# Optimization experiments

Measured on AMD Instinct MI355X. Metric: run time of the kernel, lower is better.

The kernel has to match this reference:

```python
import jax, jax.numpy as jnp
import numpy as np

NG, N, NFG, NFR, NFP, B = 4, 64, 1024, 256, 256, 2048
SCALE = 1.0 / float(np.sqrt(NFR + NFP))
EPS = 1e-5  # torch LayerNorm default


def setup_inputs() -> dict:
    key = jax.random.key(0)
    k = jax.random.split(key, 4)
    x = jax.random.normal(k[0], (B, N, NFG), dtype=jnp.float32)
    # per-graph params stacked over NG for vectorized computation
    Wt = jax.random.normal(k[1], (NG, NFR, NFG), dtype=jnp.float32) * 0.02
    bt = jnp.zeros((NG, NFR), dtype=jnp.float32)
    Wp = jax.random.normal(k[2], (NG, NFR, NFG), dtype=jnp.float32) * 0.02
    bp = jnp.zeros((NG, NFR), dtype=jnp.float32)
    Wg = jax.random.normal(k[3], (NG, NFG, NFG), dtype=jnp.float32) * 0.02  # [out,in]
    gamma = jnp.ones((NG, NFG), dtype=jnp.float32)
    beta = jnp.zeros((NG, NFG), dtype=jnp.float32)
    return {"x": x, "Wt": Wt, "bt": bt, "Wp": Wp, "bp": bp,
            "Wg": Wg, "gamma": gamma, "beta": beta}


def reference(x, Wt, bt, Wp, bp, Wg, gamma, beta):
    # theta/phi projections, vectorized over NG graphs: [G,B,N,R]
    theta = jnp.einsum('bnf,grf->gbnr', x, Wt) + bt[:, None, None, :]
    phi = jnp.einsum('bnf,grf->gbnr', x, Wp) + bp[:, None, None, :]
    # original computes sim=theta@phi^T then .sum(2); identical math:
    # relation[b,n] = theta[b,n] . sum_m phi[b,m]  (avoids the NxN matrix)
    phi_sum = phi.sum(axis=2)                                  # [G,B,R]
    relation = jnp.einsum('gbnr,gbr->gbn', theta, phi_sum) * SCALE
    w = jax.nn.softmax(relation, axis=2)                       # softmax over boxes N
    # attention-weighted aggregation over boxes -> [G,B,NFG]
    agg = jnp.einsum('gbn,bnf->gbf', w, x)
    # GCN linear (no bias): [G,B,NFG]
    h = jnp.einsum('gbf,gof->gbo', agg, Wg)
    # LayerNorm over feature dim, per graph
    mu = h.mean(axis=-1, keepdims=True)
    var = ((h - mu) ** 2).mean(axis=-1, keepdims=True)
    h = (h - mu) * jax.lax.rsqrt(var + EPS) * gamma[:, None, :] + beta[:, None, :]
    h = jax.nn.relu(h)
    # mean over the NG graphs; restore keepdim axis -> [B,1,NFG]
    return h.mean(axis=0)[:, None, :]
```

## Files before the change

### kernel.cpp

```cpp
#include <hip/hip_runtime.h>
#include <hip/hip_bf16.h>

typedef __attribute__((ext_vector_type(4))) float f4;
typedef __attribute__((ext_vector_type(4))) float f32x4;
typedef __attribute__((ext_vector_type(8))) short short8;
typedef __attribute__((ext_vector_type(2))) unsigned int u32x2;
typedef __attribute__((ext_vector_type(4))) unsigned int u32x4;
typedef unsigned int u32;
typedef unsigned short u16;

#define SCALE_F 0.04419417382415922f

__device__ inline u16 f2bf(float f) {
  u32 u = __float_as_uint(f);
  u32 r = u + 0x7FFFu + ((u >> 16) & 1u);
  return (u16)(r >> 16);
}
__device__ inline u32 pk(float a, float b) {
  return (u32)f2bf(a) | ((u32)f2bf(b) << 16);
}
__device__ inline float bflo(u32 u) { return __uint_as_float(u << 16); }
__device__ inline float bfhi(u32 u) { return __uint_as_float(u & 0xFFFF0000u); }

#define GLD16(gsrc, ldst)                                                     \
  __builtin_amdgcn_global_load_lds(                                           \
      (const __attribute__((address_space(1))) void*)(gsrc),                  \
      (__attribute__((address_space(3))) void*)(ldst), 16, 0, 0)

#define SWZ(o) (((o) & ~2047) | (((((o) >> 4) & 127) ^ (((o) >> 11) & 7)) << 4))

__device__ __forceinline__ void cvt8(const float* __restrict__ src,
                                     u16* __restrict__ dst, int blk, int t) {
  int i = blk * 256 + t;
  const f4* s = (const f4*)src;
  f4 a = s[(size_t)i * 2];
  f4 b = s[(size_t)i * 2 + 1];
  u32x4 p;
  p[0] = pk(a[0], a[1]);
  p[1] = pk(a[2], a[3]);
  p[2] = pk(b[0], b[1]);
  p[3] = pk(b[2], b[3]);
  *(u32x4*)(dst + (size_t)i * 8) = p;
}

__global__ __launch_bounds__(256) void k01_prep(const float* __restrict__ x,
                                                const float* __restrict__ Wg,
                                                const float* __restrict__ Wp,
                                                const float* __restrict__ Wt,
                                                u16* __restrict__ xs16,
                                                char* __restrict__ xpre,
                                                u16* __restrict__ wgb,
                                                u16* __restrict__ wpb,
                                                u16* __restrict__ wtb) {
  __shared__ float red[256][8];
  __shared__ u16 tile[64][66];
  const int blk = blockIdx.x, t = threadIdx.x;
  if (blk < 2048) {
    const int b = blk;
    const float* xb = x + (size_t)b * 65536;
    char* xp = xpre + (size_t)b * 131072;
    const int g16 = t & 127, rp = t >> 7;
    f4 acc0 = {0.f, 0.f, 0.f, 0.f}, acc1 = {0.f, 0.f, 0.f, 0.f};
#pragma unroll 8
    for (int it = 0; it < 32; ++it) {
      int n = it * 2 + rp;
      const float* src = xb + n * 1024 + g16 * 8;
      f4 v0 = *(const f4*)(src);
      f4 v1 = *(const f4*)(src + 4);
      acc0 += v0;
      acc1 += v1;
      u32x4 p;
      p[0] = pk(v0[0], v0[1]);
      p[1] = pk(v0[2], v0[3]);
      p[2] = pk(v1[0], v1[1]);
      p[3] = pk(v1[2], v1[3]);
      *(u32x4*)(xp + n * 2048 + g16 * 16) = p;
    }
    *(f4*)&red[t][0] = acc0;
    *(f4*)&red[t][4] = acc1;
    __syncthreads();
    if (t < 128) {
      f4 s0 = *(const f4*)&red[t][0];
      f4 s1 = *(const f4*)&red[t][4];
      f4 q0 = *(const f4*)&red[t + 128][0];
      f4 q1 = *(const f4*)&red[t + 128][4];
      s0 += q0;
      s1 += q1;
      u32x4 p;
      p[0] = pk(s0[0], s0[1]);
      p[1] = pk(s0[2], s0[3]);
      p[2] = pk(s1[0], s1[1]);
      p[3] = pk(s1[2], s1[3]);
      *(u32x4*)(xs16 + (size_t)b * 1024 + t * 8) = p;
    }
  } else if (blk < 4096) {
    cvt8(Wg, wgb, blk - 2048, t);
  } else if (blk < 4608) {
    cvt8(Wp, wpb, blk - 4096, t);
  } else {
    const int bid = blk - 4608;
    const int g = bid >> 6, rem = bid & 63;
    const int f0 = (rem & 15) * 64, r0 = (rem >> 4) * 64;
    const float* src = Wt + ((size_t)g * 256 + r0) * 1024 + f0;
#pragma unroll
    for (int i = 0; i < 16; ++i) {
      int idx = t + i * 256;
      int rl = idx >> 6, fl = idx & 63;
      tile[fl][rl] = f2bf(src[rl * 1024 + fl]);
    }
    __syncthreads();
    u16* dst = wtb + ((size_t)g * 1024 + f0) * 256 + r0;
#pragma unroll
    for (int i = 0; i < 4; ++i) {
      int idx = t + i * 256;
      int fl = idx >> 4, rq = idx & 15;
      u32x2 p;
      p[0] = (u32)tile[fl][rq * 4]     | ((u32)tile[fl][rq * 4 + 1] << 16);
      p[1] = (u32)tile[fl][rq * 4 + 2] | ((u32)tile[fl][rq * 4 + 3] << 16);
      *(u32x2*)(dst + fl * 256 + rq * 4) = p;
    }
  }
}

__global__ __launch_bounds__(256) void k2_gemm(const u16* __restrict__ A,
                                               const u16* __restrict__ Bt,
                                               const float* __restrict__ bp,
                                               u16* __restrict__ C) {
  const int n0 = blockIdx.x * 64, m0 = blockIdx.y * 128;
  __shared__ u16 Al[128 * 32];
  __shared__ u16 Bl[64 * 32];
  const int t = threadIdx.x;
  const int w = t >> 6, l = t & 63;
  const int lr = l & 15, lh = l >> 4;
  f32x4 acc[2][4] = {};
  for (int kt = 0; kt < 1024; kt += 32) {
#pragma unroll
    for (int j = 0; j < 2; ++j) {
      int idx = t + j * 256;
      int row = idx >> 2, sl = idx & 3;
      GLD16(A + (size_t)(m0 + row) * 1024 + kt + sl * 8, Al + idx * 8);
    }
    {
      int row = t >> 2, sl = t & 3;
      GLD16(Bt + (size_t)(n0 + row) * 1024 + kt + sl * 8, Bl + t * 8);
    }
    __syncthreads();
    short8 af[2], bfr[4];
#pragma unroll
    for (int m = 0; m < 2; ++m)
      af[m] = *(const short8*)(Al + (w * 32 + m * 16 + lr) * 32 + lh * 8);
#pragma unroll
    for (int n = 0; n < 4; ++n)
      bfr[n] = *(const short8*)(Bl + (n * 16 + lr) * 32 + lh * 8);
#pragma unroll
    for (int m = 0; m < 2; ++m)
#pragma unroll
      for (int n = 0; n < 4; ++n)
        acc[m][n] = __builtin_amdgcn_mfma_f32_16x16x32_bf16(af[m], bfr[n],
                                                            acc[m][n], 0, 0, 0);
    __syncthreads();
  }
#pragma unroll
  for (int m = 0; m < 2; ++m)
#pragma unroll
    for (int n = 0; n < 4; ++n) {
      int col = n0 + n * 16 + lr;
      float bb = 64.0f * bp[col];
#pragma unroll
      for (int j = 0; j < 4; ++j)
        C[(size_t)(m0 + w * 32 + m * 16 + lh * 4 + j) * 1024 + col] =
            f2bf(acc[m][n][j] + bb);
    }
}

__global__ __launch_bounds__(256) void k3_gemm(const u16* __restrict__ A,
                                               const u16* __restrict__ Btt,
                                               u16* __restrict__ Vb) {
  const int id = blockIdx.x;
  const int wg = (id & 7) * 64 + (id >> 3);
  const int n0 = (wg & 7) * 128, m0 = ((wg >> 3) & 15) * 128, g = wg >> 7;
  const u16* Bg = Btt + (size_t)g * 1024 * 256;
  __shared__ u16 Al[128 * 32];
  __shared__ u16 Bl[128 * 32];
  const int t = threadIdx.x;
  const int w = t >> 6, l = t & 63;
  const int wr = w >> 1, wc = w & 1;
  const int lr = l & 15, lh = l >> 4;
  f32x4 acc[4][4] = {};
  for (int kt = 0; kt < 256; kt += 32) {
#pragma unroll
    for (int j = 0; j < 2; ++j) {
      int idx = t + j * 256;
      int row = idx >> 2, sl = idx & 3;
      GLD16(A + (size_t)(m0 + row) * 1024 + g * 256 + kt + sl * 8, Al + idx * 8);
      GLD16(Bg + (size_t)(n0 + row) * 256 + kt + sl * 8, Bl + idx * 8);
    }
    __syncthreads();
    short8 af[4], bfr[4];
#pragma unroll
    for (int m = 0; m < 4; ++m)
      af[m] = *(const short8*)(Al + (wr * 64 + m * 16 + lr) * 32 + lh * 8);
#pragma unroll
    for (int n = 0; n < 4; ++n)
      bfr[n] = *(const short8*)(Bl + (wc * 64 + n * 16 + lr) * 32 + lh * 8);
#pragma unroll
    for (int m = 0; m < 4; ++m)
#pragma unroll
      for (int n = 0; n < 4; ++n)
        acc[m][n] = __builtin_amdgcn_mfma_f32_16x16x32_bf16(af[m], bfr[n],
                                                            acc[m][n], 0, 0, 0);
    __syncthreads();
  }
  u16* Vg = Vb + (size_t)g * 2048 * 1024;
#pragma unroll
  for (int m = 0; m < 4; ++m)
#pragma unroll
    for (int n = 0; n < 4; ++n)
#pragma unroll
      for (int j = 0; j < 4; ++j)
        Vg[(size_t)(m0 + wr * 64 + m * 16 + lh * 4 + j) * 1024 +
           (n0 + wc * 64 + n * 16 + lr)] = f2bf(acc[m][n][j]);
}

__device__ __forceinline__ void relation_phase(const char* xl, const u16* vb,
                                               float* relp, int w, int l) {
  const int lg = l >> 4, lr = l & 15;
  f32x4 racc[4] = {};
#pragma unroll
  for (int kp = 0; kp < 2; ++kp) {
    const int kt = kp * 512 + w * 32;
    short8 afr = {};
    if (lr < 4) afr = *(const short8*)(vb + lr * 1032 + kt + lg * 8);
#pragma unroll
    for (int nt = 0; nt < 4; ++nt) {
      int n = nt * 16 + lr;
      short8 bfrg = *(const short8*)(
          xl + n * 2048 + ((((kt >> 3) + lg) ^ (n & 7)) << 4));
      racc[nt] = __builtin_amdgcn_mfma_f32_16x16x32_bf16(afr, bfrg, racc[nt],
                                                         0, 0, 0);
    }
  }
  if (l < 16) {
#pragma unroll
    for (int nt = 0; nt < 4; ++nt)
#pragma unroll
      for (int j = 0; j < 4; ++j)
        relp[(w * 4 + j) * 64 + nt * 16 + lr] = racc[nt][j];
  }
}

__device__ __forceinline__ void softmax_phase(const float* relp, float* wsm,
                                              int t) {
  if (t < 256) {
    const int g = t >> 6, n = t & 63;
    float rel = 0.f;
#pragma unroll
    for (int ww = 0; ww < 16; ++ww) rel += relp[(ww * 4 + g) * 64 + n];
    rel *= SCALE_F;
    float mx = rel;
#pragma unroll
    for (int o = 32; o > 0; o >>= 1) mx = fmaxf(mx, __shfl_xor(mx, o, 64));
    float e = __expf(rel - mx);
    float s = e;
#pragma unroll
    for (int o = 32; o > 0; o >>= 1) s += __shfl_xor(s, o, 64);
    wsm[t] = e / s;
  }
}

__device__ __forceinline__ void agg_phase(const char* xl, const float* wsm,
                                          float* relp, u16* aggb, int b,
                                          int t) {
  const int hh = t >> 9, r = t & 511, g = r >> 7, f8 = r & 127;
  const float* wg = wsm + g * 64 + hh * 32;
  float a0 = 0, a1 = 0, a2 = 0, a3 = 0, a4 = 0, a5 = 0, a6 = 0, a7 = 0;
#pragma unroll 8
  for (int n0 = 0; n0 < 32; ++n0) {
    int n = hh * 32 + n0;
    float wv = wg[n0];
    u32x4 xp = *(const u32x4*)(xl + n * 2048 + ((f8 ^ (n & 7)) << 4));
    a0 = fmaf(bflo(xp[0]), wv, a0);
    a1 = fmaf(bfhi(xp[0]), wv, a1);
    a2 = fmaf(bflo(xp[1]), wv, a2);
    a3 = fmaf(bfhi(xp[1]), wv, a3);
    a4 = fmaf(bflo(xp[2]), wv, a4);
    a5 = fmaf(bfhi(xp[2]), wv, a5);
    a6 = fmaf(bflo(xp[3]), wv, a6);
    a7 = fmaf(bfhi(xp[3]), wv, a7);
  }
  if (hh) {
    f4 q0 = {a0, a1, a2, a3};
    f4 q1 = {a4, a5, a6, a7};
    *(f4*)(relp + r * 8) = q0;
    *(f4*)(relp + r * 8 + 4) = q1;
  }
  __syncthreads();
  if (!hh) {
    f4 q0 = *(const f4*)(relp + r * 8);
    f4 q1 = *(const f4*)(relp + r * 8 + 4);
    u32x4 p;
    p[0] = pk(a0 + q0[0], a1 + q0[1]);
    p[1] = pk(a2 + q0[2], a3 + q0[3]);
    p[2] = pk(a4 + q1[0], a5 + q1[1]);
    p[3] = pk(a6 + q1[2], a7 + q1[3]);
    *(u32x4*)(aggb + ((size_t)g * 2048 + b) * 1024 + f8 * 8) = p;
  }
}

#define K4_LDS (131072 + 8256 + 16384 + 1024)
__global__ __launch_bounds__(1024) void k4_fused(const char* __restrict__ xpre,
                                                 const u16* __restrict__ vb16,
                                                 u16* __restrict__ aggb) {
  extern __shared__ char sm[];
  char* xl = sm;
  u16* vb = (u16*)(sm + 131072);
  float* relp = (float*)(sm + 131072 + 8256);
  float* wsm = (float*)(sm + 131072 + 8256 + 16384);
  const int t = threadIdx.x;
  const int w = t >> 6, l = t & 63;
  const int bbase = (255 - (int)blockIdx.x) * 8;

  {
    int g = t >> 8, q = t & 255;
    u32x2 pv = *(const u32x2*)(vb16 + ((size_t)g * 2048 + bbase) * 1024 + q * 4);
    *(u32x2*)(vb + g * 1032 + q * 4) = pv;
  }
  const char* xg0 = xpre + (size_t)bbase * 131072;
#pragma unroll
  for (int i = 0; i < 8; ++i) {
    int o = (w * 8 + i) * 1024 + l * 16;
    GLD16(xg0 + SWZ(o), xl + o);
  }
  __syncthreads();

  u32x4 pf0, pf1, pf2, pf3, pf4, pf5, pf6, pf7;
  u32x2 pv1;
  for (int ib = 0; ib < 8; ++ib) {
    const int b = bbase + ib;
    if (ib < 7) {
      const char* xg1 = xpre + (size_t)(b + 1) * 131072;
      pf0 = *(const u32x4*)(xg1 + SWZ(t * 16));
      pf1 = *(const u32x4*)(xg1 + SWZ(t * 16 + 16384));
      pf2 = *(const u32x4*)(xg1 + SWZ(t * 16 + 32768));
      pf3 = *(const u32x4*)(xg1 + SWZ(t * 16 + 49152));
      pf4 = *(const u32x4*)(xg1 + SWZ(t * 16 + 65536));
      pf5 = *(const u32x4*)(xg1 + SWZ(t * 16 + 81920));
      pf6 = *(const u32x4*)(xg1 + SWZ(t * 16 + 98304));
      pf7 = *(const u32x4*)(xg1 + SWZ(t * 16 + 114688));
      pv1 = *(const u32x2*)(vb16 + ((size_t)(t >> 8) * 2048 + (b + 1)) * 1024 +
                            (t & 255) * 4);
    }
    relation_phase(xl, vb, relp, w, l);
    __syncthreads();
    softmax_phase(relp, wsm, t);
    __syncthreads();
    agg_phase(xl, wsm, relp, aggb, b, t);
    __syncthreads();
    if (ib < 7) {
      *(u32x4*)(xl + t * 16) = pf0;
      *(u32x4*)(xl + t * 16 + 16384) = pf1;
      *(u32x4*)(xl + t * 16 + 32768) = pf2;
      *(u32x4*)(xl + t * 16 + 49152) = pf3;
      *(u32x4*)(xl + t * 16 + 65536) = pf4;
      *(u32x4*)(xl + t * 16 + 81920) = pf5;
      *(u32x4*)(xl + t * 16 + 98304) = pf6;
      *(u32x4*)(xl + t * 16 + 114688) = pf7;
      *(u32x2*)(vb + (t >> 8) * 1032 + (t & 255) * 4) = pv1;
      __syncthreads();
    }
  }
}

__global__ __launch_bounds__(256) void k5_gemm(const u16* __restrict__ Ab,
                                               const u16* __restrict__ Bb,
                                               u16* __restrict__ H) {
  const int id = blockIdx.x;
  const int wg = (id & 7) * 64 + (id >> 3);
  const int n0 = (wg & 7) * 128, m0 = ((wg >> 3) & 15) * 128, g = wg >> 7;
  const u16* A = Ab + (size_t)g * 2048 * 1024;
  const u16* Bt = Bb + (size_t)g * 1024 * 1024;
  __shared__ u16 Al[128 * 32];
  __shared__ u16 Bl[128 * 32];
  const int t = threadIdx.x;
  const int w = t >> 6, l = t & 63;
  const int wr = w >> 1, wc = w & 1;
  const int lr = l & 15, lh = l >> 4;
  f32x4 acc[4][4] = {};
  for (int kt = 0; kt < 1024; kt += 32) {
#pragma unroll
    for (int j = 0; j < 2; ++j) {
      int idx = t + j * 256;
      int row = idx >> 2, sl = idx & 3;
      GLD16(A + (size_t)(m0 + row) * 1024 + kt + sl * 8, Al + idx * 8);
      GLD16(Bt + (size_t)(n0 + row) * 1024 + kt + sl * 8, Bl + idx * 8);
    }
    __syncthreads();
    short8 af[4], bfr[4];
#pragma unroll
    for (int m = 0; m < 4; ++m)
      af[m] = *(const short8*)(Al + (wr * 64 + m * 16 + lr) * 32 + lh * 8);
#pragma unroll
    for (int n = 0; n < 4; ++n)
      bfr[n] = *(const short8*)(Bl + (wc * 64 + n * 16 + lr) * 32 + lh * 8);
#pragma unroll
    for (int m = 0; m < 4; ++m)
#pragma unroll
      for (int n = 0; n < 4; ++n)
        acc[m][n] = __builtin_amdgcn_mfma_f32_16x16x32_bf16(af[m], bfr[n],
                                                            acc[m][n], 0, 0, 0);
    __syncthreads();
  }
  u16* Hg = H + (size_t)g * 2048 * 1024;
#pragma unroll
  for (int m = 0; m < 4; ++m)
#pragma unroll
    for (int n = 0; n < 4; ++n)
#pragma unroll
      for (int j = 0; j < 4; ++j)
        Hg[(size_t)(m0 + wr * 64 + m * 16 + lh * 4 + j) * 1024 +
           (n0 + wc * 64 + n * 16 + lr)] = f2bf(acc[m][n][j]);
}

__global__ __launch_bounds__(256) void k6_ln(const u16* __restrict__ H,
                                             const float* __restrict__ gamma,
                                             const float* __restrict__ beta,
                                             float* __restrict__ out) {
  const int b = blockIdx.x, t = threadIdx.x;
  const int w = t >> 6, lane = t & 63;
  __shared__ float red[8];
  f4 acc = {0.f, 0.f, 0.f, 0.f};
  for (int g = 0; g < 4; ++g) {
    u32x2 hp = *(const u32x2*)(H + ((size_t)g * 2048 + b) * 1024 + t * 4);
    f4 hv = {bflo(hp[0]), bfhi(hp[0]), bflo(hp[1]), bfhi(hp[1])};
    float s = hv[0] + hv[1] + hv[2] + hv[3];
    float q = hv[0] * hv[0] + hv[1] * hv[1] + hv[2] * hv[2] + hv[3] * hv[3];
#pragma unroll
    for (int o = 32; o > 0; o >>= 1) {
      s += __shfl_xor(s, o, 64);
      q += __shfl_xor(q, o, 64);
    }
    if (lane == 0) { red[w] = s; red[4 + w] = q; }
    __syncthreads();
    s = red[0] + red[1] + red[2] + red[3];
    q = red[4] + red[5] + red[6] + red[7];
    float mean = s * (1.f / 1024.f);
    float var = q * (1.f / 1024.f) - mean * mean;
    float rstd = rsqrtf(var + 1e-5f);
    f4 gm = *(const f4*)(gamma + g * 1024 + t * 4);
    f4 bt = *(const f4*)(beta + g * 1024 + t * 4);
#pragma unroll
    for (int j = 0; j < 4; ++j) {
      float val = (hv[j] - mean) * rstd * gm[j] + bt[j];
      acc[j] += fmaxf(val, 0.f);
    }
    __syncthreads();
  }
  acc *= 0.25f;
  *(f4*)(out + (size_t)b * 1024 + t * 4) = acc;
}

extern "C" void kernel_launch(void* const* d_in, const int* in_sizes, int n_in,
                              void* d_out, int out_size, void* d_ws, size_t ws_size,
                              hipStream_t stream) {
  const float* x     = (const float*)d_in[0];
  const float* Wt    = (const float*)d_in[1];
  const float* Wp    = (const float*)d_in[3];
  const float* bp    = (const float*)d_in[4];
  const float* Wg    = (const float*)d_in[5];
  const float* gamma = (const float*)d_in[6];
  const float* beta  = (const float*)d_in[7];
  float* out = (float*)d_out;

  char* ws = (char*)d_ws;
  u16*   xs16 = (u16*)(ws);
  u16*   ps16 = (u16*)(ws + (4u << 20));
  u16*   wpb  = (u16*)(ws + (8u << 20));
  u16*   wtb  = (u16*)(ws + (10u << 20));
  u16*   wgb  = (u16*)(ws + (12u << 20));
  u16*   vb16 = (u16*)(ws + (20u << 20));
  u16*   aggb = (u16*)(ws + (36u << 20));
  u16*   hb16 = (u16*)(ws + (52u << 20));
  char*  xpre = (char*)(ws + (68u << 20));

  hipFuncSetAttribute((const void*)k4_fused,
                      hipFuncAttributeMaxDynamicSharedMemorySize, K4_LDS);

  k01_prep<<<4864, 256, 0, stream>>>(x, Wg, Wp, Wt, xs16, xpre, wgb, wpb, wtb);
  k2_gemm<<<dim3(16, 16), 256, 0, stream>>>(xs16, wpb, bp, ps16);
  k3_gemm<<<512, 256, 0, stream>>>(ps16, wtb, vb16);
  k4_fused<<<256, 1024, K4_LDS, stream>>>(xpre, vb16, aggb);
  k5_gemm<<<512, 256, 0, stream>>>(aggb, wgb, hb16);
  k6_ln<<<2048, 256, 0, stream>>>(hb16, gamma, beta, out);
}
```

Baseline: 311.5 us.

## Drop bf16 x precopy; convert x in fused kernel, double-buffer GCN GEMM

Result: slower. 345.8 us (+11.0%).

```diff
diff --git a/kernel.cpp b/kernel.cpp
--- a/kernel.cpp
+++ b/kernel.cpp
@@ -26,8 +26,6 @@
   __builtin_amdgcn_global_load_lds(                                           \
       (const __attribute__((address_space(1))) void*)(gsrc),                  \
       (__attribute__((address_space(3))) void*)(ldst), 16, 0, 0)
-
-#define SWZ(o) (((o) & ~2047) | (((((o) >> 4) & 127) ^ (((o) >> 11) & 7)) << 4))
 
 __device__ __forceinline__ void cvt8(const float* __restrict__ src,
                                      u16* __restrict__ dst, int blk, int t) {
@@ -48,51 +46,21 @@
                                                 const float* __restrict__ Wp,
                                                 const float* __restrict__ Wt,
                                                 u16* __restrict__ xs16,
-                                                char* __restrict__ xpre,
                                                 u16* __restrict__ wgb,
                                                 u16* __restrict__ wpb,
                                                 u16* __restrict__ wtb) {
-  __shared__ float red[256][8];
   __shared__ u16 tile[64][66];
   const int blk = blockIdx.x, t = threadIdx.x;
   if (blk < 2048) {
-    const int b = blk;
-    const float* xb = x + (size_t)b * 65536;
-    char* xp = xpre + (size_t)b * 131072;
-    const int g16 = t & 127, rp = t >> 7;
-    f4 acc0 = {0.f, 0.f, 0.f, 0.f}, acc1 = {0.f, 0.f, 0.f, 0.f};
+    const float* xb = x + (size_t)blk * 65536;
+    f4 acc = {0.f, 0.f, 0.f, 0.f};
 #pragma unroll 8
-    for (int it = 0; it < 32; ++it) {
-      int n = it * 2 + rp;
-      const float* src = xb + n * 1024 + g16 * 8;
-      f4 v0 = *(const f4*)(src);
-      f4 v1 = *(const f4*)(src + 4);
-      acc0 += v0;
-      acc1 += v1;
-      u32x4 p;
-      p[0] = pk(v0[0], v0[1]);
-      p[1] = pk(v0[2], v0[3]);
-      p[2] = pk(v1[0], v1[1]);
-      p[3] = pk(v1[2], v1[3]);
-      *(u32x4*)(xp + n * 2048 + g16 * 16) = p;
-    }
-    *(f4*)&red[t][0] = acc0;
-    *(f4*)&red[t][4] = acc1;
-    __syncthreads();
-    if (t < 128) {
-      f4 s0 = *(const f4*)&red[t][0];
-      f4 s1 = *(const f4*)&red[t][4];
-      f4 q0 = *(const f4*)&red[t + 128][0];
-      f4 q1 = *(const f4*)&red[t + 128][4];
-      s0 += q0;
-      s1 += q1;
-      u32x4 p;
-      p[0] = pk(s0[0], s0[1]);
-      p[1] = pk(s0[2], s0[3]);
-      p[2] = pk(s1[0], s1[1]);
-      p[3] = pk(s1[2], s1[3]);
-      *(u32x4*)(xs16 + (size_t)b * 1024 + t * 8) = p;
-    }
+    for (int n = 0; n < 64; ++n)
+      acc += *(const f4*)(xb + n * 1024 + t * 4);
+    u32x2 p;
+    p[0] = pk(acc[0], acc[1]);
+    p[1] = pk(acc[2], acc[3]);
+    *(u32x2*)(xs16 + (size_t)blk * 1024 + t * 4) = p;
   } else if (blk < 4096) {
     cvt8(Wg, wgb, blk - 2048, t);
   } else if (blk < 4608) {
@@ -308,7 +276,7 @@
 }
 
 #define K4_LDS (131072 + 8256 + 16384 + 1024)
-__global__ __launch_bounds__(1024) void k4_fused(const char* __restrict__ xpre,
+__global__ __launch_bounds__(1024) void k4_fused(const float* __restrict__ x,
                                                  const u16* __restrict__ vb16,
                                                  u16* __restrict__ aggb) {
   extern __shared__ char sm[];
@@ -320,35 +288,37 @@
   const int w = t >> 6, l = t & 63;
   const int bbase = (255 - (int)blockIdx.x) * 8;
 
+  f4 pf[16];
+  u32x2 pv;
   {
-    int g = t >> 8, q = t & 255;
-    u32x2 pv = *(const u32x2*)(vb16 + ((size_t)g * 2048 + bbase) * 1024 + q * 4);
-    *(u32x2*)(vb + g * 1032 + q * 4) = pv;
-  }
-  const char* xg0 = xpre + (size_t)bbase * 131072;
-#pragma unroll
-  for (int i = 0; i < 8; ++i) {
-    int o = (w * 8 + i) * 1024 + l * 16;
-    GLD16(xg0 + SWZ(o), xl + o);
-  }
+    const f4* xb = (const f4*)(x + (size_t)bbase * 65536);
+#pragma unroll
+    for (int i = 0; i < 16; ++i) pf[i] = xb[i * 1024 + t];
+    pv = *(const u32x2*)(vb16 + ((size_t)(t >> 8) * 2048 + bbase) * 1024 +
+                         (t & 255) * 4);
+  }
+#pragma unroll
+  for (int i = 0; i < 16; ++i) {
+    int idx = i * 1024 + t;
+    int row = idx >> 8, col4 = idx & 255;
+    u32 p0 = pk(pf[i][0], pf[i][1]);
+    u32 p1 = pk(pf[i][2], pf[i][3]);
+    char* dst = xl + row * 2048 + ((((col4 >> 1) ^ (row & 7)) << 4)) +
+                (col4 & 1) * 8;
+    ((u32*)dst)[0] = p0;
+    ((u32*)dst)[1] = p1;
+  }
+  *(u32x2*)(vb + (t >> 8) * 1032 + (t & 255) * 4) = pv;
   __syncthreads();
 
-  u32x4 pf0, pf1, pf2, pf3, pf4, pf5, pf6, pf7;
-  u32x2 pv1;
   for (int ib = 0; ib < 8; ++ib) {
     const int b = bbase + ib;
     if (ib < 7) {
-      const char* xg1 = xpre + (size_t)(b + 1) * 131072;
-      pf0 = *(const u32x4*)(xg1 + SWZ(t * 16));
-      pf1 = *(const u32x4*)(xg1 + SWZ(t * 16 + 16384));
-      pf2 = *(const u32x4*)(xg1 + SWZ(t * 16 + 32768));
-      pf3 = *(const u32x4*)(xg1 + SWZ(t * 16 + 49152));
-      pf4 = *(const u32x4*)(xg1 + SWZ(t * 16 + 65536));
-      pf5 = *(const u32x4*)(xg1 + SWZ(t * 16 + 81920));
-      pf6 = *(const u32x4*)(xg1 + SWZ(t * 16 + 98304));
-      pf7 = *(const u32x4*)(xg1 + SWZ(t * 16 + 114688));
-      pv1 = *(const u32x2*)(vb16 + ((size_t)(t >> 8) * 2048 + (b + 1)) * 1024 +
-                            (t & 255) * 4);
+      const f4* xb1 = (const f4*)(x + (size_t)(b + 1) * 65536);
+#pragma unroll
+      for (int i = 0; i < 16; ++i) pf[i] = xb1[i * 1024 + t];
+      pv = *(const u32x2*)(vb16 + ((size_t)(t >> 8) * 2048 + (b + 1)) * 1024 +
+                           (t & 255) * 4);
     }
     relation_phase(xl, vb, relp, w, l);
     __syncthreads();
@@ -357,15 +327,18 @@
     agg_phase(xl, wsm, relp, aggb, b, t);
     __syncthreads();
     if (ib < 7) {
-      *(u32x4*)(xl + t * 16) = pf0;
-      *(u32x4*)(xl + t * 16 + 16384) = pf1;
-      *(u32x4*)(xl + t * 16 + 32768) = pf2;
-      *(u32x4*)(xl + t * 16 + 49152) = pf3;
-      *(u32x4*)(xl + t * 16 + 65536) = pf4;
-      *(u32x4*)(xl + t * 16 + 81920) = pf5;
-      *(u32x4*)(xl + t * 16 + 98304) = pf6;
-      *(u32x4*)(xl + t * 16 + 114688) = pf7;
-      *(u32x2*)(vb + (t >> 8) * 1032 + (t & 255) * 4) = pv1;
+#pragma unroll
+      for (int i = 0; i < 16; ++i) {
+        int idx = i * 1024 + t;
+        int row = idx >> 8, col4 = idx & 255;
+        u32 p0 = pk(pf[i][0], pf[i][1]);
+        u32 p1 = pk(pf[i][2], pf[i][3]);
+        char* dst = xl + row * 2048 + ((((col4 >> 1) ^ (row & 7)) << 4)) +
+                    (col4 & 1) * 8;
+        ((u32*)dst)[0] = p0;
+        ((u32*)dst)[1] = p1;
+      }
+      *(u32x2*)(vb + (t >> 8) * 1032 + (t & 255) * 4) = pv;
       __syncthreads();
     }
   }
@@ -379,37 +352,50 @@
   const int n0 = (wg & 7) * 128, m0 = ((wg >> 3) & 15) * 128, g = wg >> 7;
   const u16* A = Ab + (size_t)g * 2048 * 1024;
   const u16* Bt = Bb + (size_t)g * 1024 * 1024;
-  __shared__ u16 Al[128 * 32];
-  __shared__ u16 Bl[128 * 32];
+  __shared__ u16 Al[2][128 * 32];
+  __shared__ u16 Bl[2][128 * 32];
   const int t = threadIdx.x;
   const int w = t >> 6, l = t & 63;
   const int wr = w >> 1, wc = w & 1;
   const int lr = l & 15, lh = l >> 4;
   f32x4 acc[4][4] = {};
-  for (int kt = 0; kt < 1024; kt += 32) {
-#pragma unroll
-    for (int j = 0; j < 2; ++j) {
-      int idx = t + j * 256;
-      int row = idx >> 2, sl = idx & 3;
-      GLD16(A + (size_t)(m0 + row) * 1024 + kt + sl * 8, Al + idx * 8);
-      GLD16(Bt + (size_t)(n0 + row) * 1024 + kt + sl * 8, Bl + idx * 8);
-    }
-    __syncthreads();
+
+#define K5_STAGE(buf, kt)                                                     \
+  do {                                                                        \
+    _Pragma("unroll") for (int j = 0; j < 2; ++j) {                           \
+      int idx = t + j * 256;                                                  \
+      int row = idx >> 2, sl = idx & 3;                                       \
+      GLD16(A + (size_t)(m0 + row) * 1024 + (kt) + sl * 8,                    \
+            &Al[buf][idx * 8]);                                               \
+      GLD16(Bt + (size_t)(n0 + row) * 1024 + (kt) + sl * 8,                   \
+            &Bl[buf][idx * 8]);                                               \
+    }                                                                         \
+  } while (0)
+
+  K5_STAGE(0, 0);
+  asm volatile("s_waitcnt vmcnt(0)" ::: "memory");
+  __builtin_amdgcn_s_barrier();
+  int cur = 0;
+  for (int s = 0; s < 32; ++s) {
+    if (s < 31) K5_STAGE(cur ^ 1, (s + 1) * 32);
     short8 af[4], bfr[4];
 #pragma unroll
     for (int m = 0; m < 4; ++m)
-      af[m] = *(const short8*)(Al + (wr * 64 + m * 16 + lr) * 32 + lh * 8);
+      af[m] = *(const short8*)(&Al[cur][(wr * 64 + m * 16 + lr) * 32 + lh * 8]);
 #pragma unroll
     for (int n = 0; n < 4; ++n)
-      bfr[n] = *(const short8*)(Bl + (wc * 64 + n * 16 + lr) * 32 + lh * 8);
+      bfr[n] = *(const short8*)(&Bl[cur][(wc * 64 + n * 16 + lr) * 32 + lh * 8]);
 #pragma unroll
     for (int m = 0; m < 4; ++m)
 #pragma unroll
       for (int n = 0; n < 4; ++n)
         acc[m][n] = __builtin_amdgcn_mfma_f32_16x16x32_bf16(af[m], bfr[n],
                                                             acc[m][n], 0, 0, 0);
-    __syncthreads();
-  }
+    asm volatile("s_waitcnt vmcnt(0)" ::: "memory");
+    __builtin_amdgcn_s_barrier();
+    cur ^= 1;
+  }
+#undef K5_STAGE
   u16* Hg = H + (size_t)g * 2048 * 1024;
 #pragma unroll
   for (int m = 0; m < 4; ++m)
@@ -480,15 +466,14 @@
   u16*   vb16 = (u16*)(ws + (20u << 20));
   u16*   aggb = (u16*)(ws + (36u << 20));
   u16*   hb16 = (u16*)(ws + (52u << 20));
-  char*  xpre = (char*)(ws + (68u << 20));
 
   hipFuncSetAttribute((const void*)k4_fused,
                       hipFuncAttributeMaxDynamicSharedMemorySize, K4_LDS);
 
-  k01_prep<<<4864, 256, 0, stream>>>(x, Wg, Wp, Wt, xs16, xpre, wgb, wpb, wtb);
+  k01_prep<<<4864, 256, 0, stream>>>(x, Wg, Wp, Wt, xs16, wgb, wpb, wtb);
   k2_gemm<<<dim3(16, 16), 256, 0, stream>>>(xs16, wpb, bp, ps16);
   k3_gemm<<<512, 256, 0, stream>>>(ps16, wtb, vb16);
-  k4_fused<<<256, 1024, K4_LDS, stream>>>(xpre, vb16, aggb);
+  k4_fused<<<256, 1024, K4_LDS, stream>>>(x, vb16, aggb);
   k5_gemm<<<512, 256, 0, stream>>>(aggb, wgb, hb16);
   k6_ln<<<2048, 256, 0, stream>>>(hb16, gamma, beta, out);
 }
```
